# Kernel tuning notes

Hardware: AMD Instinct MI355X
Metric: run time of the kernel (lower is better)

## Reference

```python
import jax, jax.numpy as jnp
import numpy as np

TOP_K = 8  # num_experts_per_tok


def setup_inputs() -> dict:
    key = jax.random.key(0)
    k1, k2 = jax.random.split(key)
    hidden_states = jax.random.normal(k1, (4, 4096, 2048), dtype=jnp.float32)
    weight = jax.random.normal(k2, (128, 2048), dtype=jnp.float32) * 0.02
    return {"hidden_states": hidden_states, "weight": weight}


def reference(hidden_states, weight):
    B, S, H = hidden_states.shape
    x = hidden_states.reshape(-1, H).astype(jnp.float32)        # [T, H], T = B*S
    logits = jnp.einsum("th,eh->te", x, weight.astype(jnp.float32))  # [T, E]
    scores = jax.nn.softmax(logits, axis=-1)                    # float32 softmax
    topk_weight, topk_idx = jax.lax.top_k(scores, TOP_K)        # [T, K]
    # norm_topk_prob=True: renormalize selected probabilities
    topk_weight = topk_weight / jnp.sum(topk_weight, axis=-1, keepdims=True)
    return topk_idx, topk_weight
```

## Files before the change

kernel.cpp:

```cpp
#include <hip/hip_runtime.h>
#include <math.h>

#define T_TOKENS 16384
#define HDIM     2048
#define NEXP     128
#define TOPK     8

#define KSPLIT   4
#define KRANGE   (HDIM / KSPLIT)
#define BK       64
#define NCHW     (KRANGE / BK)
#define KPAD     72

#define F16_MIN_NORM    6.1035156e-05f
#define SPLIT_SCALE     4096.0f
#define INV_SPLIT_SCALE 2.44140625e-04f

typedef __attribute__((ext_vector_type(8))) _Float16 f16x8;
typedef __attribute__((ext_vector_type(4))) float    f32x4;
typedef __attribute__((ext_vector_type(4))) float    f32x4v;

__device__ __forceinline__ void f16split(float f, _Float16& hi, _Float16& lo) {
    _Float16 h = (_Float16)f;
    float back = (float)h;
    if (fabsf(f) < F16_MIN_NORM) { h = (_Float16)0.f; back = 0.f; }
    lo = (_Float16)((f - back) * SPLIT_SCALE);
    hi = h;
}

__global__ __launch_bounds__(256) void pack_w(const float* __restrict__ w,
                                              unsigned short* __restrict__ wp1,
                                              unsigned short* __restrict__ wp2) {
    int p = blockIdx.x * 256 + threadIdx.x;
    int lane = p & 63, nt = (p >> 6) & 7, kk = p >> 9;
    int col = lane & 15, quad = lane >> 4;
    const float* src = w + (size_t)(nt * 16 + col) * HDIM + kk * 32 + quad * 8;
    unsigned short h[8], l[8];
#pragma unroll
    for (int j = 0; j < 8; ++j) {
        _Float16 hh, ll;
        f16split(src[j], hh, ll);
        union { _Float16 x; unsigned short u; } ch, cl;
        ch.x = hh; cl.x = ll;
        h[j] = ch.u; l[j] = cl.u;
    }
    *(uint4*)(wp1 + (size_t)p * 8) = *(const uint4*)h;
    *(uint4*)(wp2 + (size_t)p * 8) = *(const uint4*)l;
}

__global__ __launch_bounds__(256, 4) void moe_gate(const float* __restrict__ x,
                                                   const unsigned short* __restrict__ wp1,
                                                   const unsigned short* __restrict__ wp2,
                                                   float* __restrict__ out_idx,
                                                   float* __restrict__ out_w) {
    __shared__ __align__(16) unsigned char smem[33792];
    float* epil = (float*)smem;

    const int tid  = threadIdx.x;
    const int lane = tid & 63;
    const int wv   = tid >> 6;
    const int col  = lane & 15;
    const int quad = lane >> 4;
    const long tok0 = (long)blockIdx.x * 16;
    const int kbase = wv * KRANGE;

    unsigned short* buf0 = (unsigned short*)(smem + wv * 4608);
    unsigned short* buf1 = (unsigned short*)(smem + wv * 4608 + 2304);

    const int srow = lane >> 2, scol = (lane & 3) * 16;
    const float* xg = x + (tok0 + srow) * HDIM + kbase + scol;
    const int woff = srow * KPAD + scol;

    f32x4 acc[8], accc[8];
#pragma unroll
    for (int n = 0; n < 8; ++n) { acc[n] = (f32x4){0,0,0,0}; accc[n] = (f32x4){0,0,0,0}; }

    for (int ch = 0; ch < NCHW; ++ch) {
        f32x4v xv[4];
#pragma unroll
        for (int j = 0; j < 4; ++j)
            xv[j] = __builtin_nontemporal_load((const f32x4v*)(xg + ch * BK + 4 * j));

        unsigned short h[16], l[16];
#pragma unroll
        for (int j = 0; j < 16; ++j) {
            _Float16 hh, ll;
            f16split(xv[j >> 2][j & 3], hh, ll);
            union { _Float16 x; unsigned short u; } ch_, cl_;
            ch_.x = hh; cl_.x = ll;
            h[j] = ch_.u; l[j] = cl_.u;
        }
        *(uint4*)(buf0 + woff)     = *(const uint4*)(h);
        *(uint4*)(buf0 + woff + 8) = *(const uint4*)(h + 8);
        *(uint4*)(buf1 + woff)     = *(const uint4*)(l);
        *(uint4*)(buf1 + woff + 8) = *(const uint4*)(l + 8);
        __builtin_amdgcn_wave_barrier();

#pragma unroll
        for (int ks = 0; ks < 2; ++ks) {
            const int kk = wv * 16 + ch * 2 + ks;
            f16x8 a1 = *(const f16x8*)(buf0 + col * KPAD + ks * 32 + quad * 8);
            f16x8 a2 = *(const f16x8*)(buf1 + col * KPAD + ks * 32 + quad * 8);
#pragma unroll
            for (int nt = 0; nt < 8; ++nt) {
                const size_t off = ((size_t)(kk * 8 + nt) * 64 + lane) * 8;
                f16x8 b1 = *(const f16x8*)(wp1 + off);
                f16x8 b2 = *(const f16x8*)(wp2 + off);
                acc[nt]  = __builtin_amdgcn_mfma_f32_16x16x32_f16(a1, b1, acc[nt],  0, 0, 0);
                accc[nt] = __builtin_amdgcn_mfma_f32_16x16x32_f16(a1, b2, accc[nt], 0, 0, 0);
                accc[nt] = __builtin_amdgcn_mfma_f32_16x16x32_f16(a2, b1, accc[nt], 0, 0, 0);
            }
        }
        __builtin_amdgcn_wave_barrier();
    }

    __syncthreads();

#pragma unroll
    for (int nt = 0; nt < 8; ++nt)
#pragma unroll
        for (int r = 0; r < 4; ++r)
            epil[(wv * 16 + quad * 4 + r) * 132 + nt * 16 + col] =
                acc[nt][r] + accc[nt][r] * INV_SPLIT_SCALE;
    __syncthreads();

    for (int i = 0; i < 4; ++i) {
        const int t = wv * 4 + i;
        float v0 = 0.f, v1 = 0.f;
#pragma unroll
        for (int q = 0; q < KSPLIT; ++q) {
            float2 p = *(const float2*)(epil + (q * 16 + t) * 132 + 2 * lane);
            v0 += p.x; v1 += p.y;
        }
        const int i0 = 2 * lane, i1 = 2 * lane + 1;

        float topv[TOPK];
        int topi[TOPK];
#pragma unroll
        for (int s = 0; s < TOPK; ++s) {
            float mv = (v0 >= v1) ? v0 : v1;
            int   mi = (v0 >= v1) ? i0 : i1;
#pragma unroll
            for (int off = 32; off >= 1; off >>= 1) {
                float ov = __shfl_xor(mv, off);
                int   oi = __shfl_xor(mi, off);
                if (ov > mv || (ov == mv && oi < mi)) { mv = ov; mi = oi; }
            }
            topv[s] = mv; topi[s] = mi;
            if (i0 == mi) v0 = -INFINITY;
            if (i1 == mi) v1 = -INFINITY;
        }

        const float m = topv[0];
        float sum = 0.f;
#pragma unroll
        for (int s = 0; s < TOPK; ++s) sum += expf(topv[s] - m);
        const float inv = 1.f / sum;

        float myv = topv[0]; int myi = topi[0];
#pragma unroll
        for (int s = 1; s < TOPK; ++s)
            if (lane == s) { myv = topv[s]; myi = topi[s]; }

        if (lane < TOPK) {
            long tok = tok0 + t;
            out_idx[tok * TOPK + lane] = (float)myi;
            out_w[tok * TOPK + lane]   = expf(myv - m) * inv;
        }
    }
}

extern "C" void kernel_launch(void* const* d_in, const int* in_sizes, int n_in,
                              void* d_out, int out_size, void* d_ws, size_t ws_size,
                              hipStream_t stream) {
    const float* x = (const float*)d_in[0];
    const float* w = (const float*)d_in[1];
    float* out = (float*)d_out;

    unsigned short* wp1 = (unsigned short*)d_ws;
    unsigned short* wp2 = wp1 + (size_t)NEXP * HDIM;

    pack_w<<<(64 * 8 * 64) / 256, 256, 0, stream>>>(w, wp1, wp2);
    moe_gate<<<T_TOKENS / 16, 256, 0, stream>>>(x, wp1, wp2, out, out + (size_t)T_TOKENS * TOPK);
}
```

Baseline: 254.6 us.

## Process 32 tokens per block and double-buffer x chunks in LDS

Each block now handles 32 tokens as two 16-row M tiles, so every weight fragment loaded from global memory feeds twice as many MFMAs. The x chunk for the next K step is loaded into registers before the MFMAs of the current chunk run, and is converted and stored to a second LDS buffer afterwards, so global load latency overlaps with compute. In exchange, accumulator and register pressure double, LDS grows to 72 KB, launch bounds drop to 2 blocks per CU, and the grid is halved, which lowers occupancy.

```diff
diff --git a/kernel.cpp b/kernel.cpp
--- a/kernel.cpp
+++ b/kernel.cpp
@@ -18,7 +18,6 @@
 
 typedef __attribute__((ext_vector_type(8))) _Float16 f16x8;
 typedef __attribute__((ext_vector_type(4))) float    f32x4;
-typedef __attribute__((ext_vector_type(4))) float    f32x4v;
 
 __device__ __forceinline__ void f16split(float f, _Float16& hi, _Float16& lo) {
     _Float16 h = (_Float16)f;
@@ -48,12 +47,12 @@
     *(uint4*)(wp2 + (size_t)p * 8) = *(const uint4*)l;
 }
 
-__global__ __launch_bounds__(256, 4) void moe_gate(const float* __restrict__ x,
+__global__ __launch_bounds__(256, 2) void moe_gate(const float* __restrict__ x,
                                                    const unsigned short* __restrict__ wp1,
                                                    const unsigned short* __restrict__ wp2,
                                                    float* __restrict__ out_idx,
                                                    float* __restrict__ out_w) {
-    __shared__ __align__(16) unsigned char smem[33792];
+    __shared__ __align__(16) unsigned char smem[73728];
     float* epil = (float*)smem;
 
     const int tid  = threadIdx.x;
@@ -61,75 +60,108 @@
     const int wv   = tid >> 6;
     const int col  = lane & 15;
     const int quad = lane >> 4;
-    const long tok0 = (long)blockIdx.x * 16;
+    const long tok0 = (long)blockIdx.x * 32;
     const int kbase = wv * KRANGE;
 
-    unsigned short* buf0 = (unsigned short*)(smem + wv * 4608);
-    unsigned short* buf1 = (unsigned short*)(smem + wv * 4608 + 2304);
-
-    const int srow = lane >> 2, scol = (lane & 3) * 16;
-    const float* xg = x + (tok0 + srow) * HDIM + kbase + scol;
-    const int woff = srow * KPAD + scol;
-
-    f32x4 acc[8], accc[8];
-#pragma unroll
-    for (int n = 0; n < 8; ++n) { acc[n] = (f32x4){0,0,0,0}; accc[n] = (f32x4){0,0,0,0}; }
+    unsigned short* bufs[2][2];
+    bufs[0][0] = (unsigned short*)(smem + wv * 18432);
+    bufs[0][1] = (unsigned short*)(smem + wv * 18432 + 4608);
+    bufs[1][0] = (unsigned short*)(smem + wv * 18432 + 9216);
+    bufs[1][1] = (unsigned short*)(smem + wv * 18432 + 13824);
+
+    const int srow = lane >> 4, sseg = lane & 15;
+    const float* xg = x + (tok0 + srow) * HDIM + kbase + sseg * 4;
+
+    f32x4 acc[2][8], accc[2][8];
+#pragma unroll
+    for (int m = 0; m < 2; ++m)
+#pragma unroll
+        for (int n = 0; n < 8; ++n) { acc[m][n] = (f32x4){0,0,0,0}; accc[m][n] = (f32x4){0,0,0,0}; }
+
+    f32x4 xv[8];
+
+    auto load_x = [&](int ch) {
+#pragma unroll
+        for (int it = 0; it < 8; ++it)
+            xv[it] = __builtin_nontemporal_load(
+                (const f32x4*)(xg + (size_t)(it * 4) * HDIM + ch * BK));
+    };
+
+    auto cvt_store = [&](int buf) {
+#pragma unroll
+        for (int it = 0; it < 8; ++it) {
+            unsigned short h[4], l[4];
+#pragma unroll
+            for (int j = 0; j < 4; ++j) {
+                _Float16 hh, ll;
+                f16split(xv[it][j], hh, ll);
+                union { _Float16 x; unsigned short u; } ch_, cl_;
+                ch_.x = hh; cl_.x = ll;
+                h[j] = ch_.u; l[j] = cl_.u;
+            }
+            const int off = (it * 4 + srow) * KPAD + sseg * 4;
+            *(uint2*)(bufs[buf][0] + off) = *(const uint2*)h;
+            *(uint2*)(bufs[buf][1] + off) = *(const uint2*)l;
+        }
+    };
+
+    load_x(0);
+    cvt_store(0);
+    __builtin_amdgcn_wave_barrier();
 
     for (int ch = 0; ch < NCHW; ++ch) {
-        f32x4v xv[4];
-#pragma unroll
-        for (int j = 0; j < 4; ++j)
-            xv[j] = __builtin_nontemporal_load((const f32x4v*)(xg + ch * BK + 4 * j));
-
-        unsigned short h[16], l[16];
-#pragma unroll
-        for (int j = 0; j < 16; ++j) {
-            _Float16 hh, ll;
-            f16split(xv[j >> 2][j & 3], hh, ll);
-            union { _Float16 x; unsigned short u; } ch_, cl_;
-            ch_.x = hh; cl_.x = ll;
-            h[j] = ch_.u; l[j] = cl_.u;
-        }
-        *(uint4*)(buf0 + woff)     = *(const uint4*)(h);
-        *(uint4*)(buf0 + woff + 8) = *(const uint4*)(h + 8);
-        *(uint4*)(buf1 + woff)     = *(const uint4*)(l);
-        *(uint4*)(buf1 + woff + 8) = *(const uint4*)(l + 8);
-        __builtin_amdgcn_wave_barrier();
+        const int cur = ch & 1;
+        if (ch + 1 < NCHW) load_x(ch + 1);
 
 #pragma unroll
         for (int ks = 0; ks < 2; ++ks) {
             const int kk = wv * 16 + ch * 2 + ks;
-            f16x8 a1 = *(const f16x8*)(buf0 + col * KPAD + ks * 32 + quad * 8);
-            f16x8 a2 = *(const f16x8*)(buf1 + col * KPAD + ks * 32 + quad * 8);
+            f16x8 b1[8], b2[8];
 #pragma unroll
             for (int nt = 0; nt < 8; ++nt) {
                 const size_t off = ((size_t)(kk * 8 + nt) * 64 + lane) * 8;
-                f16x8 b1 = *(const f16x8*)(wp1 + off);
-                f16x8 b2 = *(const f16x8*)(wp2 + off);
-                acc[nt]  = __builtin_amdgcn_mfma_f32_16x16x32_f16(a1, b1, acc[nt],  0, 0, 0);
-                accc[nt] = __builtin_amdgcn_mfma_f32_16x16x32_f16(a1, b2, accc[nt], 0, 0, 0);
-                accc[nt] = __builtin_amdgcn_mfma_f32_16x16x32_f16(a2, b1, accc[nt], 0, 0, 0);
-            }
-        }
+                b1[nt] = *(const f16x8*)(wp1 + off);
+                b2[nt] = *(const f16x8*)(wp2 + off);
+            }
+            f16x8 a1[2], a2[2];
+#pragma unroll
+            for (int m = 0; m < 2; ++m) {
+                const int ao = (m * 16 + col) * KPAD + ks * 32 + quad * 8;
+                a1[m] = *(const f16x8*)(bufs[cur][0] + ao);
+                a2[m] = *(const f16x8*)(bufs[cur][1] + ao);
+            }
+#pragma unroll
+            for (int nt = 0; nt < 8; ++nt)
+#pragma unroll
+                for (int m = 0; m < 2; ++m) {
+                    acc[m][nt]  = __builtin_amdgcn_mfma_f32_16x16x32_f16(a1[m], b1[nt], acc[m][nt],  0, 0, 0);
+                    accc[m][nt] = __builtin_amdgcn_mfma_f32_16x16x32_f16(a1[m], b2[nt], accc[m][nt], 0, 0, 0);
+                    accc[m][nt] = __builtin_amdgcn_mfma_f32_16x16x32_f16(a2[m], b1[nt], accc[m][nt], 0, 0, 0);
+                }
+        }
+
+        if (ch + 1 < NCHW) cvt_store(cur ^ 1);
         __builtin_amdgcn_wave_barrier();
     }
 
     __syncthreads();
 
 #pragma unroll
-    for (int nt = 0; nt < 8; ++nt)
-#pragma unroll
-        for (int r = 0; r < 4; ++r)
-            epil[(wv * 16 + quad * 4 + r) * 132 + nt * 16 + col] =
-                acc[nt][r] + accc[nt][r] * INV_SPLIT_SCALE;
+    for (int m = 0; m < 2; ++m)
+#pragma unroll
+        for (int nt = 0; nt < 8; ++nt)
+#pragma unroll
+            for (int r = 0; r < 4; ++r)
+                epil[((size_t)wv * 32 + m * 16 + quad * 4 + r) * 132 + nt * 16 + col] =
+                    acc[m][nt][r] + accc[m][nt][r] * INV_SPLIT_SCALE;
     __syncthreads();
 
-    for (int i = 0; i < 4; ++i) {
-        const int t = wv * 4 + i;
+    for (int i = 0; i < 8; ++i) {
+        const int t = wv * 8 + i;
         float v0 = 0.f, v1 = 0.f;
 #pragma unroll
         for (int q = 0; q < KSPLIT; ++q) {
-            float2 p = *(const float2*)(epil + (q * 16 + t) * 132 + 2 * lane);
+            float2 p = *(const float2*)(epil + ((size_t)q * 32 + t) * 132 + 2 * lane);
             v0 += p.x; v1 += p.y;
         }
         const int i0 = 2 * lane, i1 = 2 * lane + 1;
@@ -181,5 +213,5 @@
     unsigned short* wp2 = wp1 + (size_t)NEXP * HDIM;
 
     pack_w<<<(64 * 8 * 64) / 256, 256, 0, stream>>>(w, wp1, wp2);
-    moe_gate<<<T_TOKENS / 16, 256, 0, stream>>>(x, wp1, wp2, out, out + (size_t)T_TOKENS * TOPK);
-}
+    moe_gate<<<T_TOKENS / 32, 256, 0, stream>>>(x, wp1, wp2, out, out + (size_t)T_TOKENS * TOPK);
+}
```

After: 256.8 us. Within noise of the previous version (+0.9%).
